# Performance work log

Hardware: AMD Instinct MI355X
Metric: run time of the kernel (lower is better)

## Reference

```python
import jax, jax.numpy as jnp
import numpy as np

B, S, H = 1, 2048, 2048
NH, KVH, D = 32, 8, 64
G = NH // KVH  # num_key_value_groups = 4


def setup_inputs() -> dict:
    key = jax.random.key(0)
    k1, k2, k3 = jax.random.split(key, 3)
    x = jax.random.normal(k1, (B, S, H), dtype=jnp.float32)
    w_qkv = jax.random.normal(k2, ((NH + 2 * KVH) * D, H), dtype=jnp.float32) * 0.02
    w_o = jax.random.normal(k3, (H, NH * D), dtype=jnp.float32) * 0.02
    return {"x": x, "w_qkv": w_qkv, "w_o": w_o}


def _rope_cos_sin(seqlen, dim, dtype):
    inv_freq = 1.0 / (10000.0 ** (jnp.arange(0, dim, 2, dtype=jnp.float32) / dim))
    t = jnp.arange(seqlen, dtype=jnp.float32)
    freqs = jnp.outer(t, inv_freq)  # [S, D/2]
    return jnp.cos(freqs).astype(dtype), jnp.sin(freqs).astype(dtype)


def _apply_rope(x, cos, sin):
    # x: [B,S,h,D]; non-interleaved half rotation (flash-attn RotaryEmbedding)
    d2 = x.shape[-1] // 2
    x1, x2 = x[..., :d2], x[..., d2:]
    c = cos[None, :, None, :]
    s = sin[None, :, None, :]
    return jnp.concatenate([x1 * c - x2 * s, x2 * c + x1 * s], axis=-1)


def reference(x, w_qkv, w_o):
    b, s, _ = x.shape
    qkv = x @ w_qkv.T  # fused QKV proj: [B,S,(NH+2*KVH)*D]
    q, kv = jnp.split(qkv, [NH * D], axis=-1)
    q = q.reshape(b, s, NH, D)
    kv = kv.reshape(b, s, 2, KVH, D)
    cos, sin = _rope_cos_sin(s, D, x.dtype)
    q = _apply_rope(q, cos, sin)
    k = _apply_rope(kv[:, :, 0], cos, sin)
    v = kv[:, :, 1]
    # GQA: group q heads per kv head instead of repeat_interleave (same math)
    qg = q.reshape(b, s, KVH, G, D)
    scale = 1.0 / np.sqrt(D).astype(np.float32)
    scores = jnp.einsum('bskgd,btkd->bkgst', qg, k) * scale  # [B,KVH,G,S,S]
    causal = jnp.tril(jnp.ones((s, s), dtype=bool))
    scores = jnp.where(causal[None, None, None], scores, jnp.asarray(-jnp.inf, scores.dtype))
    p = jax.nn.softmax(scores, axis=-1)
    out = jnp.einsum('bkgst,btkd->bskgd', p, v).reshape(b, s, NH * D)
    return out @ w_o.T
```

## Files before the change

kernel.cpp:

```cpp
#include <hip/hip_runtime.h>


typedef __bf16 bf16_t;
typedef __attribute__((ext_vector_type(8))) __bf16 bf16x8;
typedef __attribute__((ext_vector_type(4))) __bf16 bf16x4;
typedef __attribute__((ext_vector_type(4))) float f32x4;
typedef __attribute__((ext_vector_type(2))) unsigned int u32x2;
typedef __attribute__((ext_vector_type(4))) unsigned int u32x4;

#define S_LEN 2048
#define H_DIM 2048
#define NHEAD 32
#define KVH 8
#define HD 64
#define QKV_N 3072

#define ENT_STRIDE 8320

__global__ void cast3_kernel(const float* __restrict__ x, const float* __restrict__ wq,
                             const float* __restrict__ wo, bf16_t* __restrict__ xb,
                             bf16_t* __restrict__ wqb, bf16_t* __restrict__ wob) {
  int i = blockIdx.x * blockDim.x + threadIdx.x;
  const int n1 = S_LEN * H_DIM / 4, n2 = QKV_N * H_DIM / 4, n3 = H_DIM * H_DIM / 4;
  const float* src; bf16_t* dst; int j;
  if (i < n1)           { src = x;  dst = xb;  j = i; }
  else if (i < n1 + n2) { src = wq; dst = wqb; j = i - n1; }
  else if (i < n1 + n2 + n3) { src = wo; dst = wob; j = i - n1 - n2; }
  else return;
  float4 v = ((const float4*)src)[j];
  bf16x4 o;
  o.x = (bf16_t)v.x; o.y = (bf16_t)v.y; o.z = (bf16_t)v.z; o.w = (bf16_t)v.w;
  ((bf16x4*)dst)[j] = o;
}

__device__ __forceinline__ void async_copy16(bf16_t* lds_base, const bf16_t* g) {
  __builtin_amdgcn_global_load_lds(
      (const __attribute__((address_space(1))) unsigned int*)g,
      (__attribute__((address_space(3))) unsigned int*)lds_base, 16, 0, 0);
}

#define GBM 128
#define GBN 128

template <int EPI>
__global__ __launch_bounds__(512, 4) void gemm_sk(const bf16_t* __restrict__ A,
                                                  const bf16_t* __restrict__ B,
                                                  float* __restrict__ C,
                                                  bf16_t* __restrict__ qb,
                                                  bf16_t* __restrict__ ktp,
                                                  bf16_t* __restrict__ vt2,
                                                  int M, int N, int K) {
  __shared__ __align__(16) bf16_t As[2][GBM * 64];
  __shared__ __align__(16) bf16_t Bs[2][GBM * 64];

  const int tid  = threadIdx.x;
  const int lane = tid & 63;
  const int w    = tid >> 6;
  const int wq   = w & 3;
  const int gw   = w >> 2;
  const int wm   = (wq >> 1) * 64;
  const int wn   = (wq & 1) * 64;
  const int c    = lane & 15;
  const int quad = lane >> 4;
  const int m0   = blockIdx.y * GBM;
  const int n0   = blockIdx.x * GBN;

  f32x4 acc[4][4] = {};

  const bf16_t* Ab = A + (size_t)m0 * K;
  const bf16_t* Bb = B + (size_t)n0 * K;

  int srow[2], skc[2], sb[2];
#pragma unroll
  for (int i = 0; i < 2; ++i) {
    int p = i * 512 + tid;
    srow[i] = p >> 3;
    skc[i]  = (p & 7) ^ (srow[i] & 7);
    sb[i]   = (i * 512 + w * 64) * 8;
  }

  auto stage = [&](int buf, int k0) {
#pragma unroll
    for (int i = 0; i < 2; ++i) {
      async_copy16(&As[buf][sb[i]], Ab + (size_t)srow[i] * K + k0 + skc[i] * 8);
      async_copy16(&Bs[buf][sb[i]], Bb + (size_t)srow[i] * K + k0 + skc[i] * 8);
    }
  };

  auto compute = [&](int buf) {
    bf16x8 af[4], bfr[4];
#pragma unroll
    for (int mt = 0; mt < 4; ++mt) {
      int row = wm + mt * 16 + c;
      af[mt] = *(const bf16x8*)&As[buf][(row * 8 + ((gw * 4 + quad) ^ (row & 7))) * 8];
    }
#pragma unroll
    for (int nt = 0; nt < 4; ++nt) {
      int rowb = wn + nt * 16 + c;
      bfr[nt] = *(const bf16x8*)&Bs[buf][(rowb * 8 + ((gw * 4 + quad) ^ (rowb & 7))) * 8];
    }
#pragma unroll
    for (int mt = 0; mt < 4; ++mt)
#pragma unroll
      for (int nt = 0; nt < 4; ++nt)
        acc[mt][nt] = __builtin_amdgcn_mfma_f32_16x16x32_bf16(af[mt], bfr[nt], acc[mt][nt], 0, 0, 0);
  };

  const int NI = K >> 6;
  stage(0, 0);
  int buf = 0;
  for (int it = 0; it < NI; ++it) {
    asm volatile("s_waitcnt vmcnt(0)" ::: "memory");
    __builtin_amdgcn_s_barrier();
    if (it + 1 < NI) stage(buf ^ 1, (it + 1) << 6);
    compute(buf);
    buf ^= 1;
  }

  __syncthreads();
  float* xch = (float*)&As[0][0];
  if (gw == 1) {
#pragma unroll
    for (int t16 = 0; t16 < 16; ++t16)
      *(f32x4*)&xch[wq * 4096 + (t16 * 64 + lane) * 4] = acc[t16 >> 2][t16 & 3];
  }
  __syncthreads();
  if (gw == 0) {
#pragma unroll
    for (int t16 = 0; t16 < 16; ++t16) {
      f32x4 o = *(const f32x4*)&xch[wq * 4096 + (t16 * 64 + lane) * 4];
      acc[t16 >> 2][t16 & 3] += o;
    }

    if (EPI == 0) {
#pragma unroll
      for (int mt = 0; mt < 4; ++mt)
#pragma unroll
        for (int nt = 0; nt < 4; ++nt)
#pragma unroll
          for (int reg = 0; reg < 4; ++reg) {
            int row = m0 + wm + mt * 16 + quad * 4 + reg;
            int col = n0 + wn + nt * 16 + c;
            C[(size_t)row * N + col] = acc[mt][nt][reg];
          }
    } else {
      const int colb = n0 + wn;
      if (colb < NHEAD * HD) {
        const int h = colb >> 6;
#pragma unroll
        for (int nt = 0; nt < 2; ++nt) {
          const int i = nt * 16 + c;
          const float invf = __expf(-(float)i * (9.210340371976184f / 32.0f));
#pragma unroll
          for (int mt = 0; mt < 4; ++mt)
#pragma unroll
            for (int reg = 0; reg < 4; ++reg) {
              const int s = m0 + wm + mt * 16 + quad * 4 + reg;
              float sn, cs;
              __sincosf((float)s * invf, &sn, &cs);
              const float x1 = acc[mt][nt][reg], x2 = acc[mt][nt + 2][reg];
              bf16_t* q = qb + (size_t)s * H_DIM + h * HD;
              q[i]      = (bf16_t)((x1 * cs - x2 * sn) * 0.125f);
              q[i + 32] = (bf16_t)((x2 * cs + x1 * sn) * 0.125f);
            }
        }
      } else if (colb < NHEAD * HD + KVH * HD) {
        const int kh = (colb - NHEAD * HD) >> 6;
#pragma unroll
        for (int nt = 0; nt < 2; ++nt) {
          const int i = nt * 16 + c;
          const float invf = __expf(-(float)i * (9.210340371976184f / 32.0f));
#pragma unroll
          for (int mt = 0; mt < 4; ++mt)
#pragma unroll
            for (int reg = 0; reg < 4; ++reg) {
              const int s = m0 + wm + mt * 16 + quad * 4 + reg;
              float sn, cs;
              __sincosf((float)s * invf, &sn, &cs);
              const float x1 = acc[mt][nt][reg], x2 = acc[mt][nt + 2][reg];
              bf16_t* kd = ktp + ((size_t)kh * S_LEN + s) * HD;
              kd[i]      = (bf16_t)(x1 * cs - x2 * sn);
              kd[i + 32] = (bf16_t)(x2 * cs + x1 * sn);
            }
        }
      } else {
        const int kh = (colb - NHEAD * HD - KVH * HD) >> 6;
#pragma unroll
        for (int nt = 0; nt < 4; ++nt) {
          const int d = nt * 16 + c;
#pragma unroll
          for (int mt = 0; mt < 4; ++mt) {
            const int sr = m0 + wm + mt * 16 + quad * 4;
            bf16x4 pv;
#pragma unroll
            for (int reg = 0; reg < 4; ++reg) pv[reg] = (bf16_t)acc[mt][nt][reg];
            *(bf16x4*)&vt2[((size_t)kh * HD + d) * S_LEN + sr] = pv;
          }
        }
      }
    }
  }
}

__global__ __launch_bounds__(256, 4) void flash_split(const bf16_t* __restrict__ qb,
                                                      const bf16_t* __restrict__ kt,
                                                      const bf16_t* __restrict__ vt2,
                                                      float* __restrict__ pbuf,
                                                      bf16_t* __restrict__ attn) {
  __shared__ __align__(16) bf16_t Ks[2][64 * 64];
  __shared__ __align__(16) bf16_t Vs[2][64 * 64];

  const int tid  = threadIdx.x;
  const int lane = tid & 63;
  const int w    = tid >> 6;
  const int e    = (int)gridDim.x - 1 - (int)blockIdx.x;
  const int kh   = e / 160;
  const int i    = e - kh * 160;

  int qt, t_begin, t_end;
  {
    int T;
    if (i < 16)      { qt = i;                T = (qt >> 1) + 1; t_begin = 0;                 t_end = T; }
    else if (i < 48) { int r = i - 16; qt = 16 + (r >> 1); int ck = r & 1;
                       T = (qt >> 1) + 1; t_begin = (ck * T) >> 1;      t_end = ((ck + 1) * T) >> 1; }
    else if (i < 96) { int r = i - 48; qt = 32 + r / 3;    int ck = r % 3;
                       T = (qt >> 1) + 1; t_begin = (ck * T) / 3;       t_end = ((ck + 1) * T) / 3; }
    else             { int r = i - 96; qt = 48 + (r >> 2); int ck = r & 3;
                       T = (qt >> 1) + 1; t_begin = (ck * T) >> 2;      t_end = ((ck + 1) * T) >> 2; }
  }
  const int T     = (qt >> 1) + 1;
  const int s0    = qt * 32;
  const int h     = kh * 4 + w;
  const int c     = lane & 15;
  const int quad  = lane >> 4;

  const int idx0 = (c + (quad & 1) * 32) * 4;
  const int idx1 = idx0 + 64;
  const bool hiY = quad >= 2;

  bf16x8 qf[2][2];
#pragma unroll
  for (int rf = 0; rf < 2; ++rf)
#pragma unroll
    for (int ks = 0; ks < 2; ++ks)
      qf[rf][ks] = *(const bf16x8*)(qb + (size_t)(s0 + rf * 16 + c) * H_DIM + h * HD + ks * 32 + quad * 8);

  f32x4 acc[2][4] = {};
  float lsum[2] = {0.f, 0.f};

  const bf16_t* kbase = kt + (size_t)kh * S_LEN * HD;
  const bf16_t* vbase = vt2 + (size_t)kh * HD * S_LEN;

  int srow[2], skc[2], sbase[2];
#pragma unroll
  for (int i2 = 0; i2 < 2; ++i2) {
    int chunkbase = i2 * 256 + w * 64;
    int p = chunkbase + lane;
    sbase[i2] = chunkbase * 8;
    srow[i2]  = p >> 3;
    skc[i2]   = (p & 7) ^ (srow[i2] & 7);
  }

  auto stage = [&](int buf, int tile) {
    const int t0 = tile * 64;
#pragma unroll
    for (int i2 = 0; i2 < 2; ++i2) {
      async_copy16(&Ks[buf][sbase[i2]], kbase + (size_t)(t0 + srow[i2]) * HD + skc[i2] * 8);
      async_copy16(&Vs[buf][sbase[i2]], vbase + (size_t)srow[i2] * S_LEN + t0 + skc[i2] * 8);
    }
  };

  stage(0, t_begin);
  int buf = 0;
  for (int tile = t_begin; tile < t_end; ++tile) {
    const int t0 = tile * 64;
    asm volatile("s_waitcnt vmcnt(0)" ::: "memory");
    __builtin_amdgcn_s_barrier();
    if (tile + 1 < t_end) stage(buf ^ 1, tile + 1);

    const bool masked = (tile == T - 1);

#pragma unroll
    for (int kh2 = 0; kh2 < 2; ++kh2) {
      unsigned pw[2][2][2];
#pragma unroll
      for (int kt2l = 0; kt2l < 2; ++kt2l) {
        const int kt2 = kh2 * 2 + kt2l;
        bf16x8 kf0 = *(const bf16x8*)&Ks[buf][((kt2 * 16 + c) * 8 + ((quad) ^ (c & 7))) * 8];
        bf16x8 kf1 = *(const bf16x8*)&Ks[buf][((kt2 * 16 + c) * 8 + ((4 + quad) ^ (c & 7))) * 8];
#pragma unroll
        for (int rf = 0; rf < 2; ++rf) {
          f32x4 st = {};
          __builtin_amdgcn_s_setprio(1);
          st = __builtin_amdgcn_mfma_f32_16x16x32_bf16(kf0, qf[rf][0], st, 0, 0, 0);
          st = __builtin_amdgcn_mfma_f32_16x16x32_bf16(kf1, qf[rf][1], st, 0, 0, 0);
          __builtin_amdgcn_s_setprio(0);
          const int row = s0 + rf * 16 + c;
          bf16x4 pk;
#pragma unroll
          for (int reg = 0; reg < 4; ++reg) {
            const int key = t0 + kt2 * 16 + quad * 4 + reg;
            float p = __expf(st[reg] - 8.0f);
            if (masked && key > row) p = 0.f;
            pk[reg] = (bf16_t)p;
            lsum[rf] += p;
          }
          u32x2 pv2 = __builtin_bit_cast(u32x2, pk);
          pw[rf][kt2l][0] = pv2.x;
          pw[rf][kt2l][1] = pv2.y;
        }
      }

      bf16x8 vf[4];
#pragma unroll
      for (int dt = 0; dt < 4; ++dt)
        vf[dt] = *(const bf16x8*)&Vs[buf][((dt * 16 + c) * 8 + ((kh2 * 4 + quad) ^ (c & 7))) * 8];

#pragma unroll
      for (int rf = 0; rf < 2; ++rf) {
        int lo, hi;
        u32x4 fwv;
        lo = __builtin_amdgcn_ds_bpermute(idx0, (int)pw[rf][0][0]);
        hi = __builtin_amdgcn_ds_bpermute(idx0, (int)pw[rf][1][0]);
        fwv.x = hiY ? (unsigned)hi : (unsigned)lo;
        lo = __builtin_amdgcn_ds_bpermute(idx0, (int)pw[rf][0][1]);
        hi = __builtin_amdgcn_ds_bpermute(idx0, (int)pw[rf][1][1]);
        fwv.y = hiY ? (unsigned)hi : (unsigned)lo;
        lo = __builtin_amdgcn_ds_bpermute(idx1, (int)pw[rf][0][0]);
        hi = __builtin_amdgcn_ds_bpermute(idx1, (int)pw[rf][1][0]);
        fwv.z = hiY ? (unsigned)hi : (unsigned)lo;
        lo = __builtin_amdgcn_ds_bpermute(idx1, (int)pw[rf][0][1]);
        hi = __builtin_amdgcn_ds_bpermute(idx1, (int)pw[rf][1][1]);
        fwv.w = hiY ? (unsigned)hi : (unsigned)lo;
        bf16x8 pa = __builtin_bit_cast(bf16x8, fwv);
        __builtin_amdgcn_s_setprio(1);
#pragma unroll
        for (int dt = 0; dt < 4; ++dt)
          acc[rf][dt] = __builtin_amdgcn_mfma_f32_16x16x32_bf16(pa, vf[dt], acc[rf][dt], 0, 0, 0);
        __builtin_amdgcn_s_setprio(0);
      }
    }
    buf ^= 1;
  }

#pragma unroll
  for (int rf = 0; rf < 2; ++rf) {
    lsum[rf] += __shfl_xor(lsum[rf], 16);
    lsum[rf] += __shfl_xor(lsum[rf], 32);
  }

  __syncthreads();
  if (i < 16) {
    float* lbuf = (float*)&Ks[0][0] + w * 32;
#pragma unroll
    for (int rf = 0; rf < 2; ++rf) lbuf[rf * 16 + c] = lsum[rf];
    asm volatile("s_waitcnt lgkmcnt(0)" ::: "memory");
#pragma unroll
    for (int rf = 0; rf < 2; ++rf)
#pragma unroll
      for (int reg = 0; reg < 4; ++reg) {
        const float inv = 1.0f / lbuf[rf * 16 + quad * 4 + reg];
        const int row = s0 + rf * 16 + quad * 4 + reg;
#pragma unroll
        for (int dt = 0; dt < 4; ++dt)
          attn[(size_t)row * H_DIM + h * HD + dt * 16 + c] = (bf16_t)(acc[rf][dt][reg] * inv);
      }
  } else {
    float* ent = pbuf + (size_t)e * ENT_STRIDE;
#pragma unroll
    for (int rf = 0; rf < 2; ++rf) {
#pragma unroll
      for (int dt = 0; dt < 4; ++dt)
#pragma unroll
        for (int reg = 0; reg < 4; ++reg)
          ent[w * 2048 + (rf * 16 + quad * 4 + reg) * 64 + dt * 16 + c] = acc[rf][dt][reg];
      ent[8192 + w * 32 + rf * 16 + c] = lsum[rf];
    }
  }
}

__global__ __launch_bounds__(256) void flash_reduce(const float* __restrict__ pbuf,
                                                    bf16_t* __restrict__ attn) {
  const int kh = blockIdx.x / 48;
  const int qt = 16 + (blockIdx.x % 48);
  const int b  = qt >> 4;
  int base;
  if (b == 1)      base = kh * 160 + 16 + (qt - 16) * 2;
  else if (b == 2) base = kh * 160 + 48 + (qt - 32) * 3;
  else             base = kh * 160 + 96 + (qt - 48) * 4;
  const int nch = b + 1;

  const int t   = threadIdx.x;
  const int h2  = t >> 6;
  const int row = (t >> 1) & 31;
  const int dh  = t & 1;

  f32x4 o[8] = {};
  float l = 0.f;
  for (int ci = 0; ci < nch; ++ci) {
    const float* ent = pbuf + (size_t)(base + ci) * ENT_STRIDE;
    const float* p = ent + h2 * 2048 + row * 64 + dh * 32;
#pragma unroll
    for (int j = 0; j < 8; ++j) {
      f32x4 v = ((const f32x4*)p)[j];
      o[j][0] += v[0]; o[j][1] += v[1]; o[j][2] += v[2]; o[j][3] += v[3];
    }
    l += ent[8192 + h2 * 32 + row];
  }
  const float inv = 1.0f / l;
  bf16_t* dst = attn + (size_t)(qt * 32 + row) * H_DIM + (kh * 4 + h2) * 64 + dh * 32;
#pragma unroll
  for (int j = 0; j < 8; ++j) {
    bf16x4 ov;
    ov[0] = (bf16_t)(o[j][0] * inv); ov[1] = (bf16_t)(o[j][1] * inv);
    ov[2] = (bf16_t)(o[j][2] * inv); ov[3] = (bf16_t)(o[j][3] * inv);
    *(bf16x4*)(dst + j * 4) = ov;
  }
}

extern "C" void kernel_launch(void* const* d_in, const int* in_sizes, int n_in,
                              void* d_out, int out_size, void* d_ws, size_t ws_size,
                              hipStream_t stream) {
  const float* x     = (const float*)d_in[0];
  const float* w_qkv = (const float*)d_in[1];
  const float* w_o   = (const float*)d_in[2];
  float* out = (float*)d_out;

  char* ws = (char*)d_ws;
  const size_t OVERLAY = (size_t)1280 * ENT_STRIDE * 4;
  bf16_t* x_bf    = (bf16_t*)ws;
  bf16_t* wqkv_bf = (bf16_t*)(ws + (size_t)S_LEN * H_DIM * 2);
  float*  pbuf    = (float*)ws;
  size_t off = OVERLAY;
  bf16_t* wo_bf   = (bf16_t*)(ws + off); off += (size_t)H_DIM * H_DIM * 2;
  bf16_t* q_bf    = (bf16_t*)(ws + off); off += (size_t)S_LEN * H_DIM * 2;
  bf16_t* k_t     = (bf16_t*)(ws + off); off += (size_t)KVH * S_LEN * HD * 2;
  bf16_t* v_t2    = (bf16_t*)(ws + off); off += (size_t)KVH * S_LEN * HD * 2;
  bf16_t* attn    = (bf16_t*)(ws + off); off += (size_t)S_LEN * H_DIM * 2;

  const int ntot = (S_LEN * H_DIM + QKV_N * H_DIM + H_DIM * H_DIM) / 4;
  cast3_kernel<<<(ntot + 255) / 256, 256, 0, stream>>>(x, w_qkv, w_o, x_bf, wqkv_bf, wo_bf);

  gemm_sk<1><<<dim3(QKV_N / GBN, S_LEN / GBM), 512, 0, stream>>>(
      x_bf, wqkv_bf, nullptr, q_bf, k_t, v_t2, S_LEN, QKV_N, H_DIM);

  flash_split<<<1280, 256, 0, stream>>>(q_bf, k_t, v_t2, pbuf, attn);
  flash_reduce<<<384, 256, 0, stream>>>(pbuf, attn);

  gemm_sk<0><<<dim3(H_DIM / GBN, S_LEN / GBM), 512, 0, stream>>>(
      attn, wo_bf, out, nullptr, nullptr, nullptr, S_LEN, H_DIM, H_DIM);
}
```

Baseline: 220.3 us.

## Rebalance flash split-K into ~4-tile chunks and store partials as bf16

Changes the split-KV work partition so each query tile is split into chunks of at most about four KV tiles, which gives 288 work items per KV head instead of 160 with more uniform per-block work. Only the first 8 query tiles finish in place; the rest write partials that the reduce kernel combines. Partial outputs are now stored in bf16 instead of fp32 to halve the scratch traffic. The cost is more reduction work, extra loop overhead in index decoding, and some precision loss from rounding unnormalised partial accumulators to bf16.

```diff
diff --git a/kernel.cpp b/kernel.cpp
--- a/kernel.cpp
+++ b/kernel.cpp
@@ -15,7 +15,9 @@
 #define HD 64
 #define QKV_N 3072
 
-#define ENT_STRIDE 8320
+#define NE_PER_KH 288
+#define NSPLIT_PER_KH 280
+#define ENT_BYTES 16896
 
 __global__ void cast3_kernel(const float* __restrict__ x, const float* __restrict__ wq,
                              const float* __restrict__ wo, bf16_t* __restrict__ xb,
@@ -214,21 +216,26 @@
   const int lane = tid & 63;
   const int w    = tid >> 6;
   const int e    = (int)gridDim.x - 1 - (int)blockIdx.x;
-  const int kh   = e / 160;
-  const int i    = e - kh * 160;
-
-  int qt, t_begin, t_end;
-  {
-    int T;
-    if (i < 16)      { qt = i;                T = (qt >> 1) + 1; t_begin = 0;                 t_end = T; }
-    else if (i < 48) { int r = i - 16; qt = 16 + (r >> 1); int ck = r & 1;
-                       T = (qt >> 1) + 1; t_begin = (ck * T) >> 1;      t_end = ((ck + 1) * T) >> 1; }
-    else if (i < 96) { int r = i - 48; qt = 32 + r / 3;    int ck = r % 3;
-                       T = (qt >> 1) + 1; t_begin = (ck * T) / 3;       t_end = ((ck + 1) * T) / 3; }
-    else             { int r = i - 96; qt = 48 + (r >> 2); int ck = r & 3;
-                       T = (qt >> 1) + 1; t_begin = (ck * T) >> 2;      t_end = ((ck + 1) * T) >> 2; }
-  }
-  const int T     = (qt >> 1) + 1;
+  const int kh   = e / NE_PER_KH;
+  const int j    = e - kh * NE_PER_KH;
+
+  int qt, chunk, nch;
+  if (j < 8) {
+    qt = j; chunk = 0; nch = 1;
+  } else {
+    int j2 = j - 8;
+    qt = 8;
+    for (;;) {
+      int Tq = (qt >> 1) + 1;
+      nch = (Tq + 3) >> 2;
+      if (j2 < nch) { chunk = j2; break; }
+      j2 -= nch; ++qt;
+    }
+  }
+  const int T       = (qt >> 1) + 1;
+  const int t_begin = (chunk * T) / nch;
+  const int t_end   = ((chunk + 1) * T) / nch;
+
   const int s0    = qt * 32;
   const int h     = kh * 4 + w;
   const int c     = lane & 15;
@@ -350,7 +357,7 @@
   }
 
   __syncthreads();
-  if (i < 16) {
+  if (j < 8) {
     float* lbuf = (float*)&Ks[0][0] + w * 32;
 #pragma unroll
     for (int rf = 0; rf < 2; ++rf) lbuf[rf * 16 + c] = lsum[rf];
@@ -366,29 +373,35 @@
           attn[(size_t)row * H_DIM + h * HD + dt * 16 + c] = (bf16_t)(acc[rf][dt][reg] * inv);
       }
   } else {
-    float* ent = pbuf + (size_t)e * ENT_STRIDE;
+    const int slot = kh * NSPLIT_PER_KH + (j - 8);
+    char* ent = (char*)pbuf + (size_t)slot * ENT_BYTES;
+    bf16_t* eo = (bf16_t*)ent;
+    float*  el = (float*)(ent + 16384);
 #pragma unroll
     for (int rf = 0; rf < 2; ++rf) {
 #pragma unroll
       for (int dt = 0; dt < 4; ++dt)
 #pragma unroll
         for (int reg = 0; reg < 4; ++reg)
-          ent[w * 2048 + (rf * 16 + quad * 4 + reg) * 64 + dt * 16 + c] = acc[rf][dt][reg];
-      ent[8192 + w * 32 + rf * 16 + c] = lsum[rf];
+          eo[w * 2048 + (rf * 16 + quad * 4 + reg) * 64 + dt * 16 + c] = (bf16_t)acc[rf][dt][reg];
+      el[w * 32 + rf * 16 + c] = lsum[rf];
     }
   }
 }
 
 __global__ __launch_bounds__(256) void flash_reduce(const float* __restrict__ pbuf,
                                                     bf16_t* __restrict__ attn) {
-  const int kh = blockIdx.x / 48;
-  const int qt = 16 + (blockIdx.x % 48);
-  const int b  = qt >> 4;
-  int base;
-  if (b == 1)      base = kh * 160 + 16 + (qt - 16) * 2;
-  else if (b == 2) base = kh * 160 + 48 + (qt - 32) * 3;
-  else             base = kh * 160 + 96 + (qt - 48) * 4;
-  const int nch = b + 1;
+  const int kh = blockIdx.x / 56;
+  const int qt = 8 + (blockIdx.x % 56);
+
+  int base = 0;
+  for (int q = 8; q < qt; ++q) {
+    int Tq = (q >> 1) + 1;
+    base += (Tq + 3) >> 2;
+  }
+  const int T   = (qt >> 1) + 1;
+  const int nch = (T + 3) >> 2;
+  base += kh * NSPLIT_PER_KH;
 
   const int t   = threadIdx.x;
   const int h2  = t >> 6;
@@ -398,23 +411,24 @@
   f32x4 o[8] = {};
   float l = 0.f;
   for (int ci = 0; ci < nch; ++ci) {
-    const float* ent = pbuf + (size_t)(base + ci) * ENT_STRIDE;
-    const float* p = ent + h2 * 2048 + row * 64 + dh * 32;
-#pragma unroll
-    for (int j = 0; j < 8; ++j) {
-      f32x4 v = ((const f32x4*)p)[j];
-      o[j][0] += v[0]; o[j][1] += v[1]; o[j][2] += v[2]; o[j][3] += v[3];
-    }
-    l += ent[8192 + h2 * 32 + row];
+    const char* ent = (const char*)pbuf + (size_t)(base + ci) * ENT_BYTES;
+    const bf16_t* p = (const bf16_t*)ent + h2 * 2048 + row * 64 + dh * 32;
+#pragma unroll
+    for (int jj = 0; jj < 8; ++jj) {
+      bf16x4 v = ((const bf16x4*)p)[jj];
+      o[jj][0] += (float)v[0]; o[jj][1] += (float)v[1];
+      o[jj][2] += (float)v[2]; o[jj][3] += (float)v[3];
+    }
+    l += ((const float*)(ent + 16384))[h2 * 32 + row];
   }
   const float inv = 1.0f / l;
   bf16_t* dst = attn + (size_t)(qt * 32 + row) * H_DIM + (kh * 4 + h2) * 64 + dh * 32;
 #pragma unroll
-  for (int j = 0; j < 8; ++j) {
+  for (int jj = 0; jj < 8; ++jj) {
     bf16x4 ov;
-    ov[0] = (bf16_t)(o[j][0] * inv); ov[1] = (bf16_t)(o[j][1] * inv);
-    ov[2] = (bf16_t)(o[j][2] * inv); ov[3] = (bf16_t)(o[j][3] * inv);
-    *(bf16x4*)(dst + j * 4) = ov;
+    ov[0] = (bf16_t)(o[jj][0] * inv); ov[1] = (bf16_t)(o[jj][1] * inv);
+    ov[2] = (bf16_t)(o[jj][2] * inv); ov[3] = (bf16_t)(o[jj][3] * inv);
+    *(bf16x4*)(dst + jj * 4) = ov;
   }
 }
 
@@ -427,7 +441,7 @@
   float* out = (float*)d_out;
 
   char* ws = (char*)d_ws;
-  const size_t OVERLAY = (size_t)1280 * ENT_STRIDE * 4;
+  const size_t OVERLAY = (size_t)1280 * 8320 * 4;
   bf16_t* x_bf    = (bf16_t*)ws;
   bf16_t* wqkv_bf = (bf16_t*)(ws + (size_t)S_LEN * H_DIM * 2);
   float*  pbuf    = (float*)ws;
@@ -444,8 +458,8 @@
   gemm_sk<1><<<dim3(QKV_N / GBN, S_LEN / GBM), 512, 0, stream>>>(
       x_bf, wqkv_bf, nullptr, q_bf, k_t, v_t2, S_LEN, QKV_N, H_DIM);
 
-  flash_split<<<1280, 256, 0, stream>>>(q_bf, k_t, v_t2, pbuf, attn);
-  flash_reduce<<<384, 256, 0, stream>>>(pbuf, attn);
+  flash_split<<<8 * NE_PER_KH, 256, 0, stream>>>(q_bf, k_t, v_t2, pbuf, attn);
+  flash_reduce<<<8 * 56, 256, 0, stream>>>(pbuf, attn);
 
   gemm_sk<0><<<dim3(H_DIM / GBN, S_LEN / GBM), 512, 0, stream>>>(
       attn, wo_bf, out, nullptr, nullptr, nullptr, S_LEN, H_DIM, H_DIM);
```

After: 214.5 us. 2.7% less time.
